# Kernel tuning notes

Hardware: AMD Instinct MI355X
Metric: run time of the kernel (lower is better)

Reference implementation:

```python
import jax, jax.numpy as jnp
import numpy as np

B, T = 32, 256
INPUT_DIM, TRAJ_TYPE_DIM = 10000, 32
HIDDEN, N_LAYERS, EMBED = 512, 2, 256
OUTPUT_DIM = 10000


def setup_inputs() -> dict:
    key = jax.random.key(0)
    ks = jax.random.split(key, 16)
    s = 0.05
    inp = {
        "locations": jax.random.randint(ks[0], (B, T), 0, INPUT_DIM),
        "times": jax.random.uniform(ks[1], (B, T, 1), dtype=jnp.float32),
        "labels": jax.random.randint(ks[2], (B,), 0, TRAJ_TYPE_DIM),
        "emb_table": jax.random.normal(ks[3], (INPUT_DIM, EMBED), jnp.float32) * s,
        "traj_emb": jax.random.normal(ks[4], (TRAJ_TYPE_DIM, HIDDEN * N_LAYERS), jnp.float32) * s,
        "w_ih0": jax.random.normal(ks[5], (3 * HIDDEN, EMBED + 1), jnp.float32) * s,
        "w_hh0": jax.random.normal(ks[6], (3 * HIDDEN, HIDDEN), jnp.float32) * s,
        "b_ih0": jax.random.normal(ks[7], (3 * HIDDEN,), jnp.float32) * s,
        "b_hh0": jax.random.normal(ks[8], (3 * HIDDEN,), jnp.float32) * s,
        "w_ih1": jax.random.normal(ks[9], (3 * HIDDEN, HIDDEN), jnp.float32) * s,
        "w_hh1": jax.random.normal(ks[10], (3 * HIDDEN, HIDDEN), jnp.float32) * s,
        "b_ih1": jax.random.normal(ks[11], (3 * HIDDEN,), jnp.float32) * s,
        "b_hh1": jax.random.normal(ks[12], (3 * HIDDEN,), jnp.float32) * s,
        "fc_w": jax.random.normal(ks[13], (OUTPUT_DIM + 1, HIDDEN), jnp.float32) * s,
        "fc_b": jax.random.normal(ks[14], (OUTPUT_DIM + 1,), jnp.float32) * s,
    }
    return inp


def _gru_layer(x_tbf, h0, w_ih, w_hh, b_ih, b_hh):
    # x_tbf: [T, B, F]; h0: [B, H]. Standard torch GRU cell math.
    x_gates = jnp.einsum("tbf,gf->tbg", x_tbf, w_ih) + b_ih  # [T,B,3H]

    def step(h, xg):
        hg = h @ w_hh.T + b_hh
        xr, xz, xn = jnp.split(xg, 3, axis=-1)
        hr, hz, hn = jnp.split(hg, 3, axis=-1)
        r = jax.nn.sigmoid(xr + hr)
        z = jax.nn.sigmoid(xz + hz)
        n = jnp.tanh(xn + r * hn)
        h_new = (1.0 - z) * n + z * h
        return h_new, h_new

    _, outs = jax.lax.scan(step, h0, x_gates)
    return outs  # [T, B, H]


def reference(locations, times, labels, emb_table, traj_emb,
              w_ih0, w_hh0, b_ih0, b_hh0, w_ih1, w_hh1, b_ih1, b_hh1,
              fc_w, fc_b):
    # init hidden: [B, L*H] -> flat view -> [L, B, H] (matches torch .view)
    h0 = traj_emb[labels].reshape(N_LAYERS, -1, HIDDEN)
    x = jnp.concatenate([emb_table[locations], times], axis=-1)  # [B,T,E+1]
    x = jnp.swapaxes(x, 0, 1)  # [T,B,E+1]
    x = _gru_layer(x, h0[0], w_ih0, w_hh0, b_ih0, b_hh0)
    x = _gru_layer(x, h0[1], w_ih1, w_hh1, b_ih1, b_hh1)
    out = jnp.swapaxes(x, 0, 1)  # [B,T,H]
    out = jax.nn.relu(out) @ fc_w.T + fc_b  # [B,T,OUT+1]
    location = jax.nn.log_softmax(out[:, :, :-1], axis=-1)
    time = jax.nn.sigmoid(out[:, :, -1])
    return (location, time)
```

## Files before the change

### kernel.cpp

```cpp
#include <hip/hip_runtime.h>

typedef unsigned short u16;
typedef __bf16 bf16x8 __attribute__((ext_vector_type(8)));
typedef float f32x4 __attribute__((ext_vector_type(4)));

#define DEVI __device__ __forceinline__

DEVI u16 f2b(float f) {
  union { float f; unsigned u; } c; c.f = f;
  unsigned r = c.u + 0x7FFFu + ((c.u >> 16) & 1u);
  return (u16)(r >> 16);
}

DEVI float sigm(float x) { return 1.f / (1.f + __expf(-x)); }
DEVI float tanhfast(float x) {
  x = fminf(fmaxf(x, -15.f), 15.f);
  float e = __expf(2.f * x);
  return (e - 1.f) / (e + 1.f);
}

DEVI void async16(const void* g, void* l) {
  __builtin_amdgcn_global_load_lds((const __attribute__((address_space(1))) void*)g,
                                   (__attribute__((address_space(3))) void*)l, 16, 0, 0);
}

DEVI f32x4 ld16cc(const u16* p) {
  f32x4 r;
  asm volatile("global_load_dwordx4 %0, %1, off sc0 sc1" : "=v"(r) : "v"(p) : "memory");
  return r;
}

__global__ __launch_bounds__(256) void k_castpad(const float* __restrict__ src, u16* __restrict__ dst,
                                                 int srows, int scols, int drows, int dcols) {
  size_t n = (size_t)drows * dcols;
  for (size_t i = blockIdx.x * 256 + threadIdx.x; i < n; i += (size_t)gridDim.x * 256) {
    int r = (int)(i / dcols), c = (int)(i % dcols);
    float v = (r < srows && c < scols) ? src[(size_t)r * scols + c] : 0.f;
    dst[i] = f2b(v);
  }
}

__global__ __launch_bounds__(256) void k_embed(const int* __restrict__ loc, const float* __restrict__ times,
                                               const float* __restrict__ emb, u16* __restrict__ x0) {
  int m = blockIdx.x * 4 + (threadIdx.x >> 6);
  int s = threadIdx.x & 63;
  int b = m & 31, t = m >> 5;
  int li = loc[b * 256 + t];
  const float4* er = (const float4*)(emb + (size_t)li * 256);
  u16* xr = x0 + (size_t)m * 288;
  float4 v = er[s];
  ushort4 u;
  u.x = f2b(v.x); u.y = f2b(v.y); u.z = f2b(v.z); u.w = f2b(v.w);
  *(ushort4*)(xr + s * 4) = u;
  if (s == 0) xr[256] = f2b(times[b * 256 + t]);
  else if (s <= 31) xr[256 + s] = 0;
}

__global__ __launch_bounds__(256) void k_hinit(const float* __restrict__ traj, const int* __restrict__ labels,
                                               u16* __restrict__ dst, int layer) {
  int idx = blockIdx.x * 256 + threadIdx.x;
  if (idx < 16384) {
    int fidx = layer * 16384 + idx;
    dst[idx] = f2b(traj[(size_t)labels[fidx >> 10] * 1024 + (fidx & 1023)]);
  }
}

__global__ __launch_bounds__(128) void k_taginit(unsigned* __restrict__ tag0) {
  int t = threadIdx.x;
  tag0[(t >> 5) * 259 * 32 + (t & 31)] = 1u;
}

template <int MODE>
__global__ __launch_bounds__(256) void k_gemm(const u16* __restrict__ A, const u16* __restrict__ Bw,
                                              const float* __restrict__ bias, float* __restrict__ C,
                                              int N, int K, float* __restrict__ tptr) {
  __shared__ __align__(16) u16 As[128 * 32];
  __shared__ __align__(16) u16 Bs[128 * 32];
  const int tid = threadIdx.x;
  const int lane = tid & 63, wid = tid >> 6;
  const int tn = blockIdx.x, tm = blockIdx.y;
  const int wm = wid >> 1, wn = wid & 1;

  f32x4 acc[4][4] = {};

  const int r0 = tid >> 2;
  const int cb0 = (tid * 16) & 63;

  for (int k0 = 0; k0 < K; k0 += 32) {
    __syncthreads();
#pragma unroll
    for (int p = 0; p < 2; ++p) {
      int row = r0 + p * 64;
      const u16* ga = A + (size_t)(tm * 128 + row) * K + k0 + (cb0 >> 1);
      async16(ga, (void*)(As + wid * 512 + p * 2048));
      const u16* gb = Bw + (size_t)(tn * 128 + row) * K + k0 + (cb0 >> 1);
      async16(gb, (void*)(Bs + wid * 512 + p * 2048));
    }
    asm volatile("s_waitcnt vmcnt(0)" ::: "memory");
    __syncthreads();
    bf16x8 af[4], bf[4];
#pragma unroll
    for (int i = 0; i < 4; ++i) {
      af[i] = *reinterpret_cast<const bf16x8*>(As + (wm * 64 + i * 16 + (lane & 15)) * 32 + ((lane >> 4) * 8));
      bf[i] = *reinterpret_cast<const bf16x8*>(Bs + (wn * 64 + i * 16 + (lane & 15)) * 32 + ((lane >> 4) * 8));
    }
#pragma unroll
    for (int i = 0; i < 4; ++i)
#pragma unroll
      for (int j = 0; j < 4; ++j)
        acc[i][j] = __builtin_amdgcn_mfma_f32_16x16x32_bf16(af[i], bf[j], acc[i][j], 0, 0, 0);
  }

  const int row0 = tm * 128 + wm * 64;
  const int col0 = tn * 128 + wn * 64;
#pragma unroll
  for (int i = 0; i < 4; ++i)
#pragma unroll
    for (int j = 0; j < 4; ++j)
#pragma unroll
      for (int r = 0; r < 4; ++r) {
        int row = row0 + i * 16 + ((lane >> 4) * 4) + r;
        int col = col0 + j * 16 + (lane & 15);
        float v = acc[i][j][r];
        if (MODE == 0) {
          C[(size_t)row * N + col] = v + bias[col];
        } else {
          int orow = ((row & 31) << 8) + (row >> 5);
          if (col < 10000) C[(size_t)orow * 10000 + col] = v + bias[col];
          else if (col == 10000) tptr[orow] = sigm(v + bias[col]);
        }
      }
}

__global__ __launch_bounds__(512) __attribute__((amdgpu_waves_per_eu(2, 2)))
void k_scan3(const float* __restrict__ xg0,
             const u16* __restrict__ whh0, const float* __restrict__ bhh0,
             const u16* __restrict__ wih1, const float* __restrict__ bih1,
             const u16* __restrict__ whh1, const float* __restrict__ bhh1,
             const float* __restrict__ traj, const int* __restrict__ labels,
             u16* __restrict__ h0x, u16* __restrict__ h1x, float* __restrict__ x1x,
             u16* __restrict__ h1seq, unsigned* __restrict__ tag0, unsigned* __restrict__ tag1)
{
  const int tid = threadIdx.x, bid = blockIdx.x;
  const int role = bid >> 5, blk = bid & 31;
  const int lane = tid & 63, wid = tid >> 6;
  const int rep = bid & 3;
  __shared__ float smD[2][3][16][16];
  __shared__ __align__(16) u16 xlds[24576];

  const int eb = tid >> 4, ejj = tid & 15;
  const int jg = (blk << 4) + ejj;

  const float* bhh = (role == 0) ? bhh0 : bhh1;
  int fidx = (role == 1 ? 16384 : 0) + eb * 512 + jg;
  float h_own = traj[(size_t)labels[fidx >> 10] * 1024 + (fidx & 1023)];
  const float bh_r = bhh[jg], bh_z = bhh[512 + jg], bh_n = bhh[1024 + jg];

  const int mt = (wid < 6) ? wid / 3 : 0, nt = (wid < 6) ? wid % 3 : 0;
  bf16x8 bfragH[16];
  float bX = 0.f;
  if (wid < 6) {
    const u16* wh = (role == 0) ? whh0 : whh1;
    const u16* wrow = wh + (size_t)(nt * 512 + (blk << 4) + (lane & 15)) * 512 + ((lane >> 4) * 8);
#pragma unroll
    for (int ks = 0; ks < 16; ++ks)
      bfragH[ks] = *reinterpret_cast<const bf16x8*>(wrow + ks * 32);
    if (role == 0) bX = bih1[nt * 512 + (blk << 4) + (lane & 15)];
  }
  if (role == 0) {
    for (int c = tid; c < 3072; c += 512) {
      int row = c >> 6, o16 = c & 63;
      int grow = (row >> 4) * 512 + (blk << 4) + (row & 15);
      const float4* src = (const float4*)(wih1 + (size_t)grow * 512 + o16 * 8);
      int byte = (row << 10) + ((o16 * 16) ^ ((row & 7) << 4));
      *(float4*)((char*)xlds + byte) = *src;
    }
  }
  __syncthreads();

  const u16* hsrc = (role == 0) ? h0x : h1x;
  u16* hdst = (role == 0) ? h0x : h1x;
  unsigned* mytag = (role == 0) ? tag0 : tag1;

  for (int s = 0; s < 258; ++s) {
    if (role == 0 && s == 257) break;
    const int rp = (s + 1) & 1, wp = s & 1;

    if (role == 0) {
      float gxr = 0.f, gxz = 0.f, gxn = 0.f;
      if (s < 256) {
        const float* q = xg0 + (size_t)s * 49152 + eb * 1536 + jg;
        gxr = q[0]; gxz = q[512]; gxn = q[1024];
      }
      {
        const unsigned* tp;
        if (lane < 32)       tp = tag0 + ((size_t)(rep * 259 + s)) * 32 + lane;
        else if (s >= 9)     tp = tag1 + ((size_t)(rep * 259 + (s - 6))) * 32 + (lane - 32);
        else                 tp = tag0 + ((size_t)(rep * 259 + s)) * 32 + (lane - 32);
        while (__ballot(__hip_atomic_load(tp, __ATOMIC_RELAXED, __HIP_MEMORY_SCOPE_AGENT) != 0u) != ~0ull) {}
      }
      if (wid < 6) {
        const u16* hs = hsrc + (rp << 14) + ((mt * 16 + (lane & 15)) << 9) + ((lane >> 4) * 8);
        f32x4 afr[16];
#pragma unroll
        for (int ks = 0; ks < 16; ++ks) afr[ks] = ld16cc(hs + ks * 32);
        asm volatile("s_waitcnt vmcnt(0)" ::: "memory");
        __builtin_amdgcn_sched_barrier(0);
        const int col = lane & 15, rb = (lane >> 4) << 2;
        if (s < 256) {
          f32x4 a0 = {0.f, 0.f, 0.f, 0.f}, a1 = {0.f, 0.f, 0.f, 0.f};
#pragma unroll
          for (int ks = 0; ks < 8; ++ks) {
            a0 = __builtin_amdgcn_mfma_f32_16x16x32_bf16(__builtin_bit_cast(bf16x8, afr[2 * ks]),     bfragH[2 * ks],     a0, 0, 0, 0);
            a1 = __builtin_amdgcn_mfma_f32_16x16x32_bf16(__builtin_bit_cast(bf16x8, afr[2 * ks + 1]), bfragH[2 * ks + 1], a1, 0, 0, 0);
          }
#pragma unroll
          for (int r = 0; r < 4; ++r) smD[mt][nt][rb + r][col] = a0[r] + a1[r];
        }
        if (s >= 1) {
          const char* xbase = (const char*)xlds + ((nt * 16 + col) << 10);
          const int cb = (lane >> 4) << 4;
          const int swz = ((col & 7) << 4);
          f32x4 c0 = {0.f, 0.f, 0.f, 0.f}, c1 = {0.f, 0.f, 0.f, 0.f};
#pragma unroll
          for (int ks = 0; ks < 8; ++ks) {
            bf16x8 x0 = *(const bf16x8*)(xbase + (((2 * ks) * 64 + cb) ^ swz));
            bf16x8 x1 = *(const bf16x8*)(xbase + (((2 * ks + 1) * 64 + cb) ^ swz));
            c0 = __builtin_amdgcn_mfma_f32_16x16x32_bf16(__builtin_bit_cast(bf16x8, afr[2 * ks]),     x0, c0, 0, 0, 0);
            c1 = __builtin_amdgcn_mfma_f32_16x16x32_bf16(__builtin_bit_cast(bf16x8, afr[2 * ks + 1]), x1, c1, 0, 0, 0);
          }
          float* xp = x1x + (size_t)((s - 1) & 7) * 49152;
#pragma unroll
          for (int r = 0; r < 4; ++r) {
            int ebr = mt * 16 + rb + r;
            __hip_atomic_store(xp + ((ebr * 3 + nt) << 9) + (blk << 4) + col,
                               c0[r] + c1[r] + bX, __ATOMIC_RELAXED, __HIP_MEMORY_SCOPE_AGENT);
          }
        }
      }
      __syncthreads();
      if (s < 256) {
        float Dr = smD[eb >> 4][0][eb & 15][ejj] + bh_r;
        float Dz = smD[eb >> 4][1][eb & 15][ejj] + bh_z;
        float Dn = smD[eb >> 4][2][eb & 15][ejj] + bh_n;
        float r = sigm(gxr + Dr);
        float z = sigm(gxz + Dz);
        float n = tanhfast(gxn + r * Dn);
        h_own = (1.f - z) * n + z * h_own;
        unsigned hv = f2b(h_own);
        unsigned oth = __shfl_xor(hv, 1);
        if (!(ejj & 1))
          __hip_atomic_store((unsigned*)(hdst + (wp << 14)) + (((eb << 9) + jg) >> 1),
                             hv | (oth << 16), __ATOMIC_RELAXED, __HIP_MEMORY_SCOPE_AGENT);
      }
    } else {
      if (s >= 2) {
        {
          const unsigned* tp = (lane < 32)
              ? tag0 + ((size_t)(rep * 259 + s)) * 32 + lane
              : tag1 + ((size_t)(rep * 259 + s)) * 32 + (lane - 32);
          while (__ballot(__hip_atomic_load(tp, __ATOMIC_RELAXED, __HIP_MEMORY_SCOPE_AGENT) != 0u) != ~0ull) {}
        }
        float* xp = x1x + (size_t)((s - 2) & 7) * 49152 + ((eb * 3) << 9) + jg;
        float gxr = __hip_atomic_load(xp,        __ATOMIC_RELAXED, __HIP_MEMORY_SCOPE_AGENT);
        float gxz = __hip_atomic_load(xp + 512,  __ATOMIC_RELAXED, __HIP_MEMORY_SCOPE_AGENT);
        float gxn = __hip_atomic_load(xp + 1024, __ATOMIC_RELAXED, __HIP_MEMORY_SCOPE_AGENT);
        if (wid < 6) {
          const u16* hs = hsrc + (rp << 14) + ((mt * 16 + (lane & 15)) << 9) + ((lane >> 4) * 8);
          f32x4 afr[16];
#pragma unroll
          for (int ks = 0; ks < 16; ++ks) afr[ks] = ld16cc(hs + ks * 32);
          asm volatile("s_waitcnt vmcnt(0)" ::: "memory");
          __builtin_amdgcn_sched_barrier(0);
          f32x4 a0 = {0.f, 0.f, 0.f, 0.f}, a1 = {0.f, 0.f, 0.f, 0.f};
#pragma unroll
          for (int ks = 0; ks < 8; ++ks) {
            a0 = __builtin_amdgcn_mfma_f32_16x16x32_bf16(__builtin_bit_cast(bf16x8, afr[2 * ks]),     bfragH[2 * ks],     a0, 0, 0, 0);
            a1 = __builtin_amdgcn_mfma_f32_16x16x32_bf16(__builtin_bit_cast(bf16x8, afr[2 * ks + 1]), bfragH[2 * ks + 1], a1, 0, 0, 0);
          }
          const int col = lane & 15, rb = (lane >> 4) << 2;
#pragma unroll
          for (int r = 0; r < 4; ++r) smD[mt][nt][rb + r][col] = a0[r] + a1[r];
        }
        __syncthreads();
        float Dr = smD[eb >> 4][0][eb & 15][ejj] + bh_r;
        float Dz = smD[eb >> 4][1][eb & 15][ejj] + bh_z;
        float Dn = smD[eb >> 4][2][eb & 15][ejj] + bh_n;
        float r = sigm(gxr + Dr);
        float z = sigm(gxz + Dz);
        float n = tanhfast(gxn + r * Dn);
        h_own = (1.f - z) * n + z * h_own;
        unsigned hv = f2b(h_own);
        unsigned oth = __shfl_xor(hv, 1);
        if (!(ejj & 1))
          __hip_atomic_store((unsigned*)(hdst + (wp << 14)) + (((eb << 9) + jg) >> 1),
                             hv | (oth << 16), __ATOMIC_RELAXED, __HIP_MEMORY_SCOPE_AGENT);
        h1seq[((size_t)((s - 2) * 32 + eb) << 9) + jg] = f2b(fmaxf(h_own, 0.f));
      }
    }
    asm volatile("s_waitcnt vmcnt(0)" ::: "memory");
    __syncthreads();
    if (tid == 0 && s < 257) {
#pragma unroll
      for (int r = 0; r < 4; ++r)
        __hip_atomic_store(mytag + ((size_t)(r * 259 + s + 1)) * 32 + blk, 1u,
                           __ATOMIC_RELAXED, __HIP_MEMORY_SCOPE_AGENT);
    }
  }
}

__global__ __launch_bounds__(256) void k_logsoftmax(float* __restrict__ out) {
  const int row = blockIdx.x, tid = threadIdx.x;
  float* p = out + (size_t)row * 10000;
  const int n_own = (tid < 16) ? 40 : 39;
  float v[40];
  float mx = -3.4e38f;
#pragma unroll
  for (int i = 0; i < 40; ++i)
    if (i < n_own) { v[i] = p[i * 256 + tid]; mx = fmaxf(mx, v[i]); }
  for (int o = 32; o; o >>= 1) mx = fmaxf(mx, __shfl_xor(mx, o));
  __shared__ float sm[4], ss[4];
  if ((tid & 63) == 0) sm[tid >> 6] = mx;
  __syncthreads();
  mx = fmaxf(fmaxf(sm[0], sm[1]), fmaxf(sm[2], sm[3]));
  float s = 0.f;
#pragma unroll
  for (int i = 0; i < 40; ++i)
    if (i < n_own) s += __expf(v[i] - mx);
  for (int o = 32; o; o >>= 1) s += __shfl_xor(s, o);
  if ((tid & 63) == 0) ss[tid >> 6] = s;
  __syncthreads();
  s = ss[0] + ss[1] + ss[2] + ss[3];
  float lse = mx + __logf(s);
#pragma unroll
  for (int i = 0; i < 40; ++i)
    if (i < n_own) p[i * 256 + tid] = v[i] - lse;
}

extern "C" void kernel_launch(void* const* d_in, const int* in_sizes, int n_in,
                              void* d_out, int out_size, void* d_ws, size_t ws_size,
                              hipStream_t stream) {
  (void)in_sizes; (void)n_in; (void)out_size;
  const int*   loc    = (const int*)  d_in[0];
  const float* times  = (const float*)d_in[1];
  const int*   labels = (const int*)  d_in[2];
  const float* emb    = (const float*)d_in[3];
  const float* traj   = (const float*)d_in[4];
  const float* w_ih0  = (const float*)d_in[5];
  const float* w_hh0  = (const float*)d_in[6];
  const float* b_ih0  = (const float*)d_in[7];
  const float* b_hh0  = (const float*)d_in[8];
  const float* w_ih1  = (const float*)d_in[9];
  const float* w_hh1  = (const float*)d_in[10];
  const float* b_ih1  = (const float*)d_in[11];
  const float* b_hh1  = (const float*)d_in[12];
  const float* fc_w   = (const float*)d_in[13];
  const float* fc_b   = (const float*)d_in[14];

  if (ws_size < 32000000) return;

  char* ws = (char*)d_ws;
  size_t off = 0;
  auto alloc = [&](size_t b) { size_t r = off; off += (b + 255) & ~(size_t)255; return r; };
  unsigned* tag0 = (unsigned*)(ws + alloc(4 * 259 * 32 * 4));
  unsigned* tag1 = (unsigned*)(ws + alloc(4 * 259 * 32 * 4));
  u16*   h0x   = (u16*)  (ws + alloc(2 * 32 * 512 * 2));
  u16*   h1x   = (u16*)  (ws + alloc(2 * 32 * 512 * 2));
  float* x1x   = (float*)(ws + alloc((size_t)8 * 32 * 3 * 512 * 4));
  u16*   x0    = (u16*)  (ws + alloc((size_t)8192 * 288 * 2));
  u16*   wih0b = (u16*)  (ws + alloc((size_t)1536 * 288 * 2));
  u16*   whh0b = (u16*)  (ws + alloc((size_t)1536 * 512 * 2));
  u16*   wih1b = (u16*)  (ws + alloc((size_t)1536 * 512 * 2));
  u16*   whh1b = (u16*)  (ws + alloc((size_t)1536 * 512 * 2));
  u16*   fcwb  = (u16*)  (ws + alloc((size_t)10112 * 512 * 2));
  u16*   h1seq = (u16*)  (ws + alloc((size_t)8192 * 512 * 2));

  float* outp = (float*)d_out;
  float* xg0  = outp;
  float* tptr = outp + 81920000;

  hipMemsetAsync(tag0, 0, 2 * 4 * 259 * 32 * 4, stream);
  k_taginit<<<1, 128, 0, stream>>>(tag0);
  k_castpad<<<1024, 256, 0, stream>>>(w_ih0, wih0b, 1536, 257, 1536, 288);
  k_castpad<<<1024, 256, 0, stream>>>(w_hh0, whh0b, 1536, 512, 1536, 512);
  k_castpad<<<1024, 256, 0, stream>>>(w_ih1, wih1b, 1536, 512, 1536, 512);
  k_castpad<<<1024, 256, 0, stream>>>(w_hh1, whh1b, 1536, 512, 1536, 512);
  k_castpad<<<1024, 256, 0, stream>>>(fc_w, fcwb, 10001, 512, 10112, 512);
  k_embed<<<2048, 256, 0, stream>>>(loc, times, emb, x0);
  k_gemm<0><<<dim3(12, 64), 256, 0, stream>>>(x0, wih0b, b_ih0, xg0, 1536, 288, nullptr);
  k_hinit<<<64, 256, 0, stream>>>(traj, labels, h0x + 16384, 0);
  k_hinit<<<64, 256, 0, stream>>>(traj, labels, h1x + 16384, 1);
  k_scan3<<<64, 512, 0, stream>>>(xg0, whh0b, b_hh0, wih1b, b_ih1, whh1b, b_hh1,
                                  traj, labels, h0x, h1x, x1x, h1seq, tag0, tag1);
  k_gemm<1><<<dim3(79, 64), 256, 0, stream>>>(h1seq, fcwb, fc_b, outp, 10112, 512, tptr);
  k_logsoftmax<<<8192, 256, 0, stream>>>(outp);
}
```

Measured before the change: 1.735 ms.

## Merge both GRU layer scans into one 32-block kernel with bitmask barrier

```diff
diff --git a/kernel.cpp b/kernel.cpp
--- a/kernel.cpp
+++ b/kernel.cpp
@@ -24,11 +24,16 @@
                                    (__attribute__((address_space(3))) void*)l, 16, 0, 0);
 }
 
-DEVI f32x4 ld16cc(const u16* p) {
-  f32x4 r;
-  asm volatile("global_load_dwordx4 %0, %1, off sc0 sc1" : "=v"(r) : "v"(p) : "memory");
-  return r;
-}
+DEVI float ldf_p(const float* p) { float r; asm volatile("global_load_dword %0, %1, off"         : "=v"(r) : "v"(p) : "memory"); return r; }
+DEVI float ldf_g(const float* p) { float r; asm volatile("global_load_dword %0, %1, off sc0 sc1" : "=v"(r) : "v"(p) : "memory"); return r; }
+DEVI f32x4 ld16_g(const u16* p)  { f32x4 r; asm volatile("global_load_dwordx4 %0, %1, off sc0 sc1" : "=v"(r) : "v"(p) : "memory"); return r; }
+DEVI void  st32_g(unsigned* p, unsigned v) { asm volatile("global_store_dword %0, %1, off sc0 sc1" :: "v"(p), "v"(v) : "memory"); }
+DEVI void  stf_g(float* p, float v)        { asm volatile("global_store_dword %0, %1, off sc0 sc1" :: "v"(p), "v"(v) : "memory"); }
+
+#define VM0 asm volatile("s_waitcnt vmcnt(0)" ::: "memory")
+#define LK0 asm volatile("s_waitcnt lgkmcnt(0)" ::: "memory")
+#define SBAR __builtin_amdgcn_sched_barrier(0)
+#define BAR __builtin_amdgcn_s_barrier()
 
 __global__ __launch_bounds__(256) void k_castpad(const float* __restrict__ src, u16* __restrict__ dst,
                                                  int srows, int scols, int drows, int dcols) {
@@ -65,9 +70,8 @@
   }
 }
 
-__global__ __launch_bounds__(128) void k_taginit(unsigned* __restrict__ tag0) {
-  int t = threadIdx.x;
-  tag0[(t >> 5) * 259 * 32 + (t & 31)] = 1u;
+__global__ __launch_bounds__(64) void k_maskinit(unsigned* __restrict__ msk) {
+  if (threadIdx.x == 0) msk[0] = 0xFFFFFFFFu;
 }
 
 template <int MODE>
@@ -132,179 +136,175 @@
       }
 }
 
-__global__ __launch_bounds__(512) __attribute__((amdgpu_waves_per_eu(2, 2)))
-void k_scan3(const float* __restrict__ xg0,
+__global__ __launch_bounds__(512, 2)
+void k_scan5(const float* __restrict__ xg0,
              const u16* __restrict__ whh0, const float* __restrict__ bhh0,
              const u16* __restrict__ wih1, const float* __restrict__ bih1,
              const u16* __restrict__ whh1, const float* __restrict__ bhh1,
              const float* __restrict__ traj, const int* __restrict__ labels,
              u16* __restrict__ h0x, u16* __restrict__ h1x, float* __restrict__ x1x,
-             u16* __restrict__ h1seq, unsigned* __restrict__ tag0, unsigned* __restrict__ tag1)
+             u16* __restrict__ h1seq, unsigned* __restrict__ msk)
 {
-  const int tid = threadIdx.x, bid = blockIdx.x;
-  const int role = bid >> 5, blk = bid & 31;
+  extern __shared__ __align__(16) char dynlds[];
+  float* smD = (float*)(dynlds + 147456);
+
+  const int tid = threadIdx.x, blk = blockIdx.x;
   const int lane = tid & 63, wid = tid >> 6;
-  const int rep = bid & 3;
-  __shared__ float smD[2][3][16][16];
-  __shared__ __align__(16) u16 xlds[24576];
-
   const int eb = tid >> 4, ejj = tid & 15;
   const int jg = (blk << 4) + ejj;
 
-  const float* bhh = (role == 0) ? bhh0 : bhh1;
-  int fidx = (role == 1 ? 16384 : 0) + eb * 512 + jg;
-  float h_own = traj[(size_t)labels[fidx >> 10] * 1024 + (fidx & 1023)];
-  const float bh_r = bhh[jg], bh_z = bhh[512 + jg], bh_n = bhh[1024 + jg];
-
-  const int mt = (wid < 6) ? wid / 3 : 0, nt = (wid < 6) ? wid % 3 : 0;
-  bf16x8 bfragH[16];
-  float bX = 0.f;
-  if (wid < 6) {
-    const u16* wh = (role == 0) ? whh0 : whh1;
-    const u16* wrow = wh + (size_t)(nt * 512 + (blk << 4) + (lane & 15)) * 512 + ((lane >> 4) * 8);
-#pragma unroll
-    for (int ks = 0; ks < 16; ++ks)
-      bfragH[ks] = *reinterpret_cast<const bf16x8*>(wrow + ks * 32);
-    if (role == 0) bX = bih1[nt * 512 + (blk << 4) + (lane & 15)];
-  }
-  if (role == 0) {
+#pragma unroll
+  for (int m = 0; m < 3; ++m) {
+    const u16* srcm = (m == 0) ? whh0 : (m == 1) ? wih1 : whh1;
+    char* dst = dynlds + m * 49152;
     for (int c = tid; c < 3072; c += 512) {
       int row = c >> 6, o16 = c & 63;
       int grow = (row >> 4) * 512 + (blk << 4) + (row & 15);
-      const float4* src = (const float4*)(wih1 + (size_t)grow * 512 + o16 * 8);
+      const float4* src = (const float4*)(srcm + (size_t)grow * 512 + o16 * 8);
       int byte = (row << 10) + ((o16 * 16) ^ ((row & 7) << 4));
-      *(float4*)((char*)xlds + byte) = *src;
-    }
-  }
+      *(float4*)(dst + byte) = *src;
+    }
+  }
+
+  float h0_own, h1_own;
+  {
+    int f0 = eb * 512 + jg;
+    h0_own = traj[(size_t)labels[f0 >> 10] * 1024 + (f0 & 1023)];
+    int f1 = 16384 + eb * 512 + jg;
+    h1_own = traj[(size_t)labels[f1 >> 10] * 1024 + (f1 & 1023)];
+  }
+  const float b0r = bhh0[jg], b0z = bhh0[512 + jg], b0n = bhh0[1024 + jg];
+  const float b1r = bhh1[jg], b1z = bhh1[512 + jg], b1n = bhh1[1024 + jg];
+
+  const int mt = (wid < 6) ? wid / 3 : 0, nt = (wid < 6) ? wid % 3 : 0;
+  float bX = 0.f;
+  if (wid < 6) bX = bih1[nt * 512 + (blk << 4) + (lane & 15)];
+
   __syncthreads();
 
-  const u16* hsrc = (role == 0) ? h0x : h1x;
-  u16* hdst = (role == 0) ? h0x : h1x;
-  unsigned* mytag = (role == 0) ? tag0 : tag1;
-
-  for (int s = 0; s < 258; ++s) {
-    if (role == 0 && s == 257) break;
-    const int rp = (s + 1) & 1, wp = s & 1;
-
-    if (role == 0) {
-      float gxr = 0.f, gxz = 0.f, gxn = 0.f;
-      if (s < 256) {
-        const float* q = xg0 + (size_t)s * 49152 + eb * 1536 + jg;
-        gxr = q[0]; gxz = q[512]; gxn = q[1024];
-      }
-      {
-        const unsigned* tp;
-        if (lane < 32)       tp = tag0 + ((size_t)(rep * 259 + s)) * 32 + lane;
-        else if (s >= 9)     tp = tag1 + ((size_t)(rep * 259 + (s - 6))) * 32 + (lane - 32);
-        else                 tp = tag0 + ((size_t)(rep * 259 + s)) * 32 + (lane - 32);
-        while (__ballot(__hip_atomic_load(tp, __ATOMIC_RELAXED, __HIP_MEMORY_SCOPE_AGENT) != 0u) != ~0ull) {}
-      }
-      if (wid < 6) {
-        const u16* hs = hsrc + (rp << 14) + ((mt * 16 + (lane & 15)) << 9) + ((lane >> 4) * 8);
-        f32x4 afr[16];
-#pragma unroll
-        for (int ks = 0; ks < 16; ++ks) afr[ks] = ld16cc(hs + ks * 32);
-        asm volatile("s_waitcnt vmcnt(0)" ::: "memory");
-        __builtin_amdgcn_sched_barrier(0);
-        const int col = lane & 15, rb = (lane >> 4) << 2;
-        if (s < 256) {
-          f32x4 a0 = {0.f, 0.f, 0.f, 0.f}, a1 = {0.f, 0.f, 0.f, 0.f};
-#pragma unroll
-          for (int ks = 0; ks < 8; ++ks) {
-            a0 = __builtin_amdgcn_mfma_f32_16x16x32_bf16(__builtin_bit_cast(bf16x8, afr[2 * ks]),     bfragH[2 * ks],     a0, 0, 0, 0);
-            a1 = __builtin_amdgcn_mfma_f32_16x16x32_bf16(__builtin_bit_cast(bf16x8, afr[2 * ks + 1]), bfragH[2 * ks + 1], a1, 0, 0, 0);
-          }
-#pragma unroll
-          for (int r = 0; r < 4; ++r) smD[mt][nt][rb + r][col] = a0[r] + a1[r];
-        }
-        if (s >= 1) {
-          const char* xbase = (const char*)xlds + ((nt * 16 + col) << 10);
-          const int cb = (lane >> 4) << 4;
-          const int swz = ((col & 7) << 4);
-          f32x4 c0 = {0.f, 0.f, 0.f, 0.f}, c1 = {0.f, 0.f, 0.f, 0.f};
-#pragma unroll
-          for (int ks = 0; ks < 8; ++ks) {
-            bf16x8 x0 = *(const bf16x8*)(xbase + (((2 * ks) * 64 + cb) ^ swz));
-            bf16x8 x1 = *(const bf16x8*)(xbase + (((2 * ks + 1) * 64 + cb) ^ swz));
-            c0 = __builtin_amdgcn_mfma_f32_16x16x32_bf16(__builtin_bit_cast(bf16x8, afr[2 * ks]),     x0, c0, 0, 0, 0);
-            c1 = __builtin_amdgcn_mfma_f32_16x16x32_bf16(__builtin_bit_cast(bf16x8, afr[2 * ks + 1]), x1, c1, 0, 0, 0);
-          }
-          float* xp = x1x + (size_t)((s - 1) & 7) * 49152;
-#pragma unroll
-          for (int r = 0; r < 4; ++r) {
-            int ebr = mt * 16 + rb + r;
-            __hip_atomic_store(xp + ((ebr * 3 + nt) << 9) + (blk << 4) + col,
-                               c0[r] + c1[r] + bX, __ATOMIC_RELAXED, __HIP_MEMORY_SCOPE_AGENT);
-          }
-        }
-      }
-      __syncthreads();
-      if (s < 256) {
-        float Dr = smD[eb >> 4][0][eb & 15][ejj] + bh_r;
-        float Dz = smD[eb >> 4][1][eb & 15][ejj] + bh_z;
-        float Dn = smD[eb >> 4][2][eb & 15][ejj] + bh_n;
-        float r = sigm(gxr + Dr);
-        float z = sigm(gxz + Dz);
-        float n = tanhfast(gxn + r * Dn);
-        h_own = (1.f - z) * n + z * h_own;
-        unsigned hv = f2b(h_own);
-        unsigned oth = __shfl_xor(hv, 1);
-        if (!(ejj & 1))
-          __hip_atomic_store((unsigned*)(hdst + (wp << 14)) + (((eb << 9) + jg) >> 1),
-                             hv | (oth << 16), __ATOMIC_RELAXED, __HIP_MEMORY_SCOPE_AGENT);
-      }
-    } else {
-      if (s >= 2) {
-        {
-          const unsigned* tp = (lane < 32)
-              ? tag0 + ((size_t)(rep * 259 + s)) * 32 + lane
-              : tag1 + ((size_t)(rep * 259 + s)) * 32 + (lane - 32);
-          while (__ballot(__hip_atomic_load(tp, __ATOMIC_RELAXED, __HIP_MEMORY_SCOPE_AGENT) != 0u) != ~0ull) {}
-        }
-        float* xp = x1x + (size_t)((s - 2) & 7) * 49152 + ((eb * 3) << 9) + jg;
-        float gxr = __hip_atomic_load(xp,        __ATOMIC_RELAXED, __HIP_MEMORY_SCOPE_AGENT);
-        float gxz = __hip_atomic_load(xp + 512,  __ATOMIC_RELAXED, __HIP_MEMORY_SCOPE_AGENT);
-        float gxn = __hip_atomic_load(xp + 1024, __ATOMIC_RELAXED, __HIP_MEMORY_SCOPE_AGENT);
-        if (wid < 6) {
-          const u16* hs = hsrc + (rp << 14) + ((mt * 16 + (lane & 15)) << 9) + ((lane >> 4) * 8);
-          f32x4 afr[16];
-#pragma unroll
-          for (int ks = 0; ks < 16; ++ks) afr[ks] = ld16cc(hs + ks * 32);
-          asm volatile("s_waitcnt vmcnt(0)" ::: "memory");
-          __builtin_amdgcn_sched_barrier(0);
-          f32x4 a0 = {0.f, 0.f, 0.f, 0.f}, a1 = {0.f, 0.f, 0.f, 0.f};
-#pragma unroll
-          for (int ks = 0; ks < 8; ++ks) {
-            a0 = __builtin_amdgcn_mfma_f32_16x16x32_bf16(__builtin_bit_cast(bf16x8, afr[2 * ks]),     bfragH[2 * ks],     a0, 0, 0, 0);
-            a1 = __builtin_amdgcn_mfma_f32_16x16x32_bf16(__builtin_bit_cast(bf16x8, afr[2 * ks + 1]), bfragH[2 * ks + 1], a1, 0, 0, 0);
-          }
-          const int col = lane & 15, rb = (lane >> 4) << 2;
-#pragma unroll
-          for (int r = 0; r < 4; ++r) smD[mt][nt][rb + r][col] = a0[r] + a1[r];
-        }
-        __syncthreads();
-        float Dr = smD[eb >> 4][0][eb & 15][ejj] + bh_r;
-        float Dz = smD[eb >> 4][1][eb & 15][ejj] + bh_z;
-        float Dn = smD[eb >> 4][2][eb & 15][ejj] + bh_n;
-        float r = sigm(gxr + Dr);
-        float z = sigm(gxz + Dz);
-        float n = tanhfast(gxn + r * Dn);
-        h_own = (1.f - z) * n + z * h_own;
-        unsigned hv = f2b(h_own);
-        unsigned oth = __shfl_xor(hv, 1);
-        if (!(ejj & 1))
-          __hip_atomic_store((unsigned*)(hdst + (wp << 14)) + (((eb << 9) + jg) >> 1),
-                             hv | (oth << 16), __ATOMIC_RELAXED, __HIP_MEMORY_SCOPE_AGENT);
-        h1seq[((size_t)((s - 2) * 32 + eb) << 9) + jg] = f2b(fmaxf(h_own, 0.f));
-      }
-    }
-    asm volatile("s_waitcnt vmcnt(0)" ::: "memory");
-    __syncthreads();
-    if (tid == 0 && s < 257) {
-#pragma unroll
-      for (int r = 0; r < 4; ++r)
-        __hip_atomic_store(mytag + ((size_t)(r * 259 + s + 1)) * 32 + blk, 1u,
-                           __ATOMIC_RELAXED, __HIP_MEMORY_SCOPE_AGENT);
+  float gxr = 0.f, gxz = 0.f, gxn = 0.f;
+  float g1r = 0.f, g1z = 0.f, g1n = 0.f;
+  {
+    const float* q = xg0 + (size_t)eb * 1536 + jg;
+    gxr = ldf_p(q); gxz = ldf_p(q + 512); gxn = ldf_p(q + 1024);
+  }
+
+  for (int s = 0; s <= 258; ++s) {
+    const int rp0 = (s + 1) & 1;
+    const int wp0 = s & 1;
+    const int rp1 = s & 1;
+    const int wp1 = (s + 1) & 1;
+
+    if (wid == 7) {
+      const unsigned* mp = msk + (size_t)s * 32;
+      while (__hip_atomic_load(mp, __ATOMIC_RELAXED, __HIP_MEMORY_SCOPE_AGENT) != 0xFFFFFFFFu)
+        __builtin_amdgcn_s_sleep(1);
+    }
+    BAR;
+
+    if (wid < 6) {
+      const int col = lane & 15, rb = (lane >> 4) << 2;
+      f32x4 afrA[16], afrB[16];
+      if (s <= 256) {
+        const u16* hs = h0x + (rp0 << 14) + ((mt * 16 + col) << 9) + ((lane >> 4) * 8);
+#pragma unroll
+        for (int ks = 0; ks < 16; ++ks) afrA[ks] = ld16_g(hs + ks * 32);
+      }
+      if (s >= 3) {
+        const u16* hs = h1x + (rp1 << 14) + ((mt * 16 + col) << 9) + ((lane >> 4) * 8);
+#pragma unroll
+        for (int ks = 0; ks < 16; ++ks) afrB[ks] = ld16_g(hs + ks * 32);
+      }
+      VM0; SBAR;
+      const int cb = (lane >> 4) << 4;
+      const int swz = ((col & 7) << 4);
+      const int rowoff = (nt * 16 + col) << 10;
+      if (s <= 255) {
+        f32x4 a0 = {0.f, 0.f, 0.f, 0.f}, a1 = {0.f, 0.f, 0.f, 0.f};
+#pragma unroll
+        for (int ks = 0; ks < 8; ++ks) {
+          bf16x8 w0 = *(const bf16x8*)(dynlds + rowoff + (((2 * ks) * 64 + cb) ^ swz));
+          bf16x8 w1 = *(const bf16x8*)(dynlds + rowoff + (((2 * ks + 1) * 64 + cb) ^ swz));
+          a0 = __builtin_amdgcn_mfma_f32_16x16x32_bf16(__builtin_bit_cast(bf16x8, afrA[2 * ks]),     w0, a0, 0, 0, 0);
+          a1 = __builtin_amdgcn_mfma_f32_16x16x32_bf16(__builtin_bit_cast(bf16x8, afrA[2 * ks + 1]), w1, a1, 0, 0, 0);
+        }
+#pragma unroll
+        for (int r = 0; r < 4; ++r)
+          smD[((0 + mt) * 3 + nt) * 256 + (rb + r) * 16 + col] = a0[r] + a1[r];
+      }
+      if (s >= 1 && s <= 256) {
+        f32x4 c0 = {0.f, 0.f, 0.f, 0.f}, c1 = {0.f, 0.f, 0.f, 0.f};
+#pragma unroll
+        for (int ks = 0; ks < 8; ++ks) {
+          bf16x8 w0 = *(const bf16x8*)(dynlds + 49152 + rowoff + (((2 * ks) * 64 + cb) ^ swz));
+          bf16x8 w1 = *(const bf16x8*)(dynlds + 49152 + rowoff + (((2 * ks + 1) * 64 + cb) ^ swz));
+          c0 = __builtin_amdgcn_mfma_f32_16x16x32_bf16(__builtin_bit_cast(bf16x8, afrA[2 * ks]),     w0, c0, 0, 0, 0);
+          c1 = __builtin_amdgcn_mfma_f32_16x16x32_bf16(__builtin_bit_cast(bf16x8, afrA[2 * ks + 1]), w1, c1, 0, 0, 0);
+        }
+        float* xp = x1x + (size_t)((s - 1) & 3) * 49152;
+#pragma unroll
+        for (int r = 0; r < 4; ++r) {
+          int ebr = mt * 16 + rb + r;
+          stf_g(xp + ((ebr * 3 + nt) << 9) + (blk << 4) + col, c0[r] + c1[r] + bX);
+        }
+      }
+      if (s >= 3) {
+        f32x4 d0 = {0.f, 0.f, 0.f, 0.f}, d1 = {0.f, 0.f, 0.f, 0.f};
+#pragma unroll
+        for (int ks = 0; ks < 8; ++ks) {
+          bf16x8 w0 = *(const bf16x8*)(dynlds + 98304 + rowoff + (((2 * ks) * 64 + cb) ^ swz));
+          bf16x8 w1 = *(const bf16x8*)(dynlds + 98304 + rowoff + (((2 * ks + 1) * 64 + cb) ^ swz));
+          d0 = __builtin_amdgcn_mfma_f32_16x16x32_bf16(__builtin_bit_cast(bf16x8, afrB[2 * ks]),     w0, d0, 0, 0, 0);
+          d1 = __builtin_amdgcn_mfma_f32_16x16x32_bf16(__builtin_bit_cast(bf16x8, afrB[2 * ks + 1]), w1, d1, 0, 0, 0);
+        }
+#pragma unroll
+        for (int r = 0; r < 4; ++r)
+          smD[((2 + mt) * 3 + nt) * 256 + (rb + r) * 16 + col] = d0[r] + d1[r];
+      }
+      LK0;
+    }
+    SBAR; BAR;
+    if (wid >= 6) { VM0; SBAR; }
+    if (s <= 255) {
+      float Dr = smD[((0 + (eb >> 4)) * 3 + 0) * 256 + (eb & 15) * 16 + ejj] + b0r;
+      float Dz = smD[((0 + (eb >> 4)) * 3 + 1) * 256 + (eb & 15) * 16 + ejj] + b0z;
+      float Dn = smD[((0 + (eb >> 4)) * 3 + 2) * 256 + (eb & 15) * 16 + ejj] + b0n;
+      float r = sigm(gxr + Dr);
+      float z = sigm(gxz + Dz);
+      float n = tanhfast(gxn + r * Dn);
+      h0_own = (1.f - z) * n + z * h0_own;
+      unsigned hv = f2b(h0_own);
+      unsigned oth = __shfl_xor(hv, 1);
+      if (!(ejj & 1))
+        st32_g((unsigned*)(h0x + (wp0 << 14)) + (((eb << 9) + jg) >> 1), hv | (oth << 16));
+    }
+    if (s >= 3) {
+      const int t = s - 3;
+      float Dr = smD[((2 + (eb >> 4)) * 3 + 0) * 256 + (eb & 15) * 16 + ejj] + b1r;
+      float Dz = smD[((2 + (eb >> 4)) * 3 + 1) * 256 + (eb & 15) * 16 + ejj] + b1z;
+      float Dn = smD[((2 + (eb >> 4)) * 3 + 2) * 256 + (eb & 15) * 16 + ejj] + b1n;
+      float r = sigm(g1r + Dr);
+      float z = sigm(g1z + Dz);
+      float n = tanhfast(g1n + r * Dn);
+      h1_own = (1.f - z) * n + z * h1_own;
+      unsigned hv = f2b(h1_own);
+      unsigned oth = __shfl_xor(hv, 1);
+      if (!(ejj & 1))
+        st32_g((unsigned*)(h1x + (wp1 << 14)) + (((eb << 9) + jg) >> 1), hv | (oth << 16));
+      h1seq[((size_t)(t * 32 + eb) << 9) + jg] = f2b(fmaxf(h1_own, 0.f));
+    }
+    VM0;
+    SBAR; BAR;
+    if (tid == 384 && s < 258)
+      __hip_atomic_fetch_or(msk + (size_t)(s + 1) * 32, 1u << blk,
+                            __ATOMIC_RELAXED, __HIP_MEMORY_SCOPE_AGENT);
+    if (s <= 254) {
+      const float* q = xg0 + (size_t)(s + 1) * 49152 + eb * 1536 + jg;
+      gxr = ldf_p(q); gxz = ldf_p(q + 512); gxn = ldf_p(q + 1024);
+    }
+    if (s >= 2 && s <= 257) {
+      const float* xc = x1x + (size_t)((s - 2) & 3) * 49152 + ((eb * 3) << 9) + jg;
+      g1r = ldf_g(xc); g1z = ldf_g(xc + 512); g1n = ldf_g(xc + 1024);
     }
   }
 }
@@ -357,16 +357,15 @@
   const float* fc_w   = (const float*)d_in[13];
   const float* fc_b   = (const float*)d_in[14];
 
-  if (ws_size < 32000000) return;
+  if (ws_size < 31500000) return;
 
   char* ws = (char*)d_ws;
   size_t off = 0;
   auto alloc = [&](size_t b) { size_t r = off; off += (b + 255) & ~(size_t)255; return r; };
-  unsigned* tag0 = (unsigned*)(ws + alloc(4 * 259 * 32 * 4));
-  unsigned* tag1 = (unsigned*)(ws + alloc(4 * 259 * 32 * 4));
+  unsigned* msk  = (unsigned*)(ws + alloc(259 * 32 * 4));
   u16*   h0x   = (u16*)  (ws + alloc(2 * 32 * 512 * 2));
   u16*   h1x   = (u16*)  (ws + alloc(2 * 32 * 512 * 2));
-  float* x1x   = (float*)(ws + alloc((size_t)8 * 32 * 3 * 512 * 4));
+  float* x1x   = (float*)(ws + alloc((size_t)4 * 32 * 3 * 512 * 4));
   u16*   x0    = (u16*)  (ws + alloc((size_t)8192 * 288 * 2));
   u16*   wih0b = (u16*)  (ws + alloc((size_t)1536 * 288 * 2));
   u16*   whh0b = (u16*)  (ws + alloc((size_t)1536 * 512 * 2));
@@ -379,8 +378,10 @@
   float* xg0  = outp;
   float* tptr = outp + 81920000;
 
-  hipMemsetAsync(tag0, 0, 2 * 4 * 259 * 32 * 4, stream);
-  k_taginit<<<1, 128, 0, stream>>>(tag0);
+  hipFuncSetAttribute((const void*)k_scan5, hipFuncAttributeMaxDynamicSharedMemorySize, 159744);
+
+  hipMemsetAsync(msk, 0, 259 * 32 * 4, stream);
+  k_maskinit<<<1, 64, 0, stream>>>(msk);
   k_castpad<<<1024, 256, 0, stream>>>(w_ih0, wih0b, 1536, 257, 1536, 288);
   k_castpad<<<1024, 256, 0, stream>>>(w_hh0, whh0b, 1536, 512, 1536, 512);
   k_castpad<<<1024, 256, 0, stream>>>(w_ih1, wih1b, 1536, 512, 1536, 512);
@@ -390,8 +391,8 @@
   k_gemm<0><<<dim3(12, 64), 256, 0, stream>>>(x0, wih0b, b_ih0, xg0, 1536, 288, nullptr);
   k_hinit<<<64, 256, 0, stream>>>(traj, labels, h0x + 16384, 0);
   k_hinit<<<64, 256, 0, stream>>>(traj, labels, h1x + 16384, 1);
-  k_scan3<<<64, 512, 0, stream>>>(xg0, whh0b, b_hh0, wih1b, b_ih1, whh1b, b_hh1,
-                                  traj, labels, h0x, h1x, x1x, h1seq, tag0, tag1);
+  k_scan5<<<32, 512, 159744, stream>>>(xg0, whh0b, b_hh0, wih1b, b_ih1, whh1b, b_hh1,
+                                       traj, labels, h0x, h1x, x1x, h1seq, msk);
   k_gemm<1><<<dim3(79, 64), 256, 0, stream>>>(h1seq, fcwb, fc_b, outp, 10112, 512, tptr);
   k_logsoftmax<<<8192, 256, 0, stream>>>(outp);
 }
```

After: 2.640 ms. 52.1% more time.
